# Kernel tuning notes

Hardware: AMD Instinct MI355X
Metric: run time of the kernel (lower is better)

Reference implementation:

```python
import jax, jax.numpy as jnp
import numpy as np
from jax import lax

HID, FFN, NUM_EXPERTS, TOP_K = 1024, 4096, 16, 4
B, S = 4, 2048


def setup_inputs() -> dict:
    key = jax.random.key(0)
    ks = jax.random.split(key, 7)
    scale = 0.02
    x = jax.random.normal(ks[0], (B, S, HID), dtype=jnp.float32)
    Wg = jax.random.normal(ks[1], (HID, NUM_EXPERTS), dtype=jnp.float32) * scale
    bg = jnp.zeros((NUM_EXPERTS,), dtype=jnp.float32)
    W1 = jax.random.normal(ks[2], (NUM_EXPERTS, HID, FFN), dtype=jnp.float32) * scale
    b1 = jnp.zeros((NUM_EXPERTS, FFN), dtype=jnp.float32)
    W2 = jax.random.normal(ks[3], (NUM_EXPERTS, FFN, HID), dtype=jnp.float32) * scale
    b2 = jnp.zeros((NUM_EXPERTS, HID), dtype=jnp.float32)
    return {"x": x, "Wg": Wg, "bg": bg, "W1": W1, "b1": b1, "W2": W2, "b2": b2}


def reference(x, Wg, bg, W1, b1, W2, b2):
    b, s, h = x.shape
    xf = x.reshape(-1, h)                                  # [T, H]
    T = xf.shape[0]
    logits = xf @ Wg + bg                                  # [T, E]
    top_w, top_idx = lax.top_k(logits, TOP_K)              # [T, K]
    top_w = jax.nn.softmax(top_w, axis=-1)
    # Dense combine weights [T, E]; topk indices are distinct so add == set.
    combine = jnp.zeros((T, NUM_EXPERTS), dtype=xf.dtype)
    combine = combine.at[jnp.arange(T)[:, None], top_idx].add(top_w)

    def body(acc, params):
        W1e, b1e, W2e, b2e, ce = params                    # ce: [T]
        hdn = jax.nn.gelu(xf @ W1e + b1e, approximate=False)  # [T, F]
        ye = hdn @ W2e + b2e                               # [T, H]
        return acc + ce[:, None] * ye, None

    out, _ = lax.scan(body, jnp.zeros_like(xf), (W1, b1, W2, b2, combine.T))
    return out.reshape(b, s, h)
```

## Files before the change

### kernel.cpp

```cpp
#include <hip/hip_runtime.h>
#include <hip/hip_bf16.h>


#define HID 1024
#define FFN 4096
#define NE 16
#define TOPK 4
#define NTOK 8192
#define NPAIR (NTOK*TOPK)

typedef __attribute__((ext_vector_type(4))) float f32x4;
typedef __attribute__((ext_vector_type(8))) short bf16x8;
typedef unsigned short u16;
typedef unsigned int u32;

__device__ __forceinline__ u16 f2bf(float f){
  u32 u = __float_as_uint(f);
  u32 r = (u + 0x7fffu + ((u >> 16) & 1u)) >> 16;
  return (u16)r;
}

__device__ __forceinline__ void gload_lds16(const void* g, void* l){
  __builtin_amdgcn_global_load_lds((const __attribute__((address_space(1))) void*)g,
                                   (__attribute__((address_space(3))) void*)l, 16, 0, 0);
}

__global__ __launch_bounds__(256) void k_gating(const float* __restrict__ x,
    const float* __restrict__ Wg, const float* __restrict__ bg,
    int* __restrict__ counts, int* __restrict__ tke, float* __restrict__ tkw,
    u16* __restrict__ xb){
  int t    = (blockIdx.x << 2) + (threadIdx.x >> 6);
  int lane = threadIdx.x & 63;
  const float* xr = x + (size_t)t*HID + lane*16;
  const float4* p = (const float4*)xr;
  float4 va = p[0], vb = p[1], vc = p[2], vd = p[3];
  float xv[16] = {va.x,va.y,va.z,va.w, vb.x,vb.y,vb.z,vb.w,
                  vc.x,vc.y,vc.z,vc.w, vd.x,vd.y,vd.z,vd.w};
  float acc[NE];
  #pragma unroll
  for (int e=0;e<NE;e++) acc[e] = 0.f;
  #pragma unroll
  for (int j=0;j<16;j++){
    const float* wr = Wg + (size_t)(lane*16 + j)*NE;
    #pragma unroll
    for (int e=0;e<NE;e++) acc[e] += xv[j] * wr[e];
  }
  uint4 o0, o1;
  o0.x = (u32)f2bf(xv[0])  | ((u32)f2bf(xv[1])  << 16);
  o0.y = (u32)f2bf(xv[2])  | ((u32)f2bf(xv[3])  << 16);
  o0.z = (u32)f2bf(xv[4])  | ((u32)f2bf(xv[5])  << 16);
  o0.w = (u32)f2bf(xv[6])  | ((u32)f2bf(xv[7])  << 16);
  o1.x = (u32)f2bf(xv[8])  | ((u32)f2bf(xv[9])  << 16);
  o1.y = (u32)f2bf(xv[10]) | ((u32)f2bf(xv[11]) << 16);
  o1.z = (u32)f2bf(xv[12]) | ((u32)f2bf(xv[13]) << 16);
  o1.w = (u32)f2bf(xv[14]) | ((u32)f2bf(xv[15]) << 16);
  u16* xbr = xb + (size_t)t*HID + lane*16;
  *(uint4*)xbr       = o0;
  *(uint4*)(xbr + 8) = o1;

  #pragma unroll
  for (int off=32; off; off>>=1){
    #pragma unroll
    for (int e=0;e<NE;e++) acc[e] += __shfl_xor(acc[e], off);
  }
  if (lane == 0){
    #pragma unroll
    for (int e=0;e<NE;e++) acc[e] += bg[e];
    int te[TOPK]; float tv[TOPK];
    #pragma unroll
    for (int k=0;k<TOPK;k++){
      int bi = 0; float bv = -1e30f;
      #pragma unroll
      for (int e=0;e<NE;e++) if (acc[e] > bv){ bv = acc[e]; bi = e; }
      te[k] = bi; tv[k] = bv; acc[bi] = -1e30f;
    }
    float m = tv[0], s = 0.f, w[TOPK];
    #pragma unroll
    for (int k=0;k<TOPK;k++){ w[k] = expf(tv[k]-m); s += w[k]; }
    float inv = 1.f/s;
    #pragma unroll
    for (int k=0;k<TOPK;k++){
      tke[t*TOPK+k] = te[k];
      tkw[t*TOPK+k] = w[k]*inv;
      atomicAdd(&counts[te[k]], 1);
    }
  }
}

__global__ __launch_bounds__(256) void k_scatter(const int* __restrict__ tke,
    const float* __restrict__ tkw, const int* __restrict__ counts,
    int* __restrict__ offsets, int* __restrict__ cursors,
    int* __restrict__ ltok, float* __restrict__ lw){
  __shared__ int loff[NE+1];
  if (threadIdx.x == 0){
    int a = 0;
    for (int e=0;e<NE;e++){ loff[e] = a; a += counts[e]; }
    loff[NE] = a;
    if (blockIdx.x == 0){
      for (int e=0;e<=NE;e++) offsets[e] = loff[e];
    }
  }
  __syncthreads();
  int t = blockIdx.x*256 + threadIdx.x;
  #pragma unroll
  for (int k=0;k<TOPK;k++){
    int e = tke[t*TOPK+k];
    int p = atomicAdd(&cursors[e], 1);
    int r = loff[e] + p;
    ltok[r] = t;
    lw[r]   = tkw[t*TOPK+k];
  }
}

__global__ __launch_bounds__(256) void k_wcvt(const float* __restrict__ src,
    u16* __restrict__ dst, int R, int C){
  int ntR = R >> 6, ntC = C >> 7;
  int ntiles = NE * ntR * ntC;
  __shared__ u16 t[64][136];
  int tid = threadIdx.x;
  for (int tile = blockIdx.x; tile < ntiles; tile += gridDim.x){
    int e   = tile / (ntR*ntC);
    int rem = tile % (ntR*ntC);
    int rt  = rem / ntC, ct = rem % ntC;
    const float* s = src + (size_t)e*R*C + (size_t)(rt*64)*C + ct*128;
    u16*         d = dst + (size_t)e*R*C + (size_t)(ct*128)*R + rt*64;
    #pragma unroll
    for (int it=0; it<8; it++){
      int i  = it*256 + tid;
      int rr = i >> 5;
      int c4 = (i & 31) << 2;
      float4 v = *(const float4*)(s + (size_t)rr*C + c4);
      t[rr][c4+0] = f2bf(v.x);
      t[rr][c4+1] = f2bf(v.y);
      t[rr][c4+2] = f2bf(v.z);
      t[rr][c4+3] = f2bf(v.w);
    }
    __syncthreads();
    #pragma unroll
    for (int it=0; it<4; it++){
      int i   = it*256 + tid;
      int cc  = i >> 3;
      int rr0 = (i & 7) << 3;
      uint4 o;
      o.x = (u32)t[rr0+0][cc] | ((u32)t[rr0+1][cc] << 16);
      o.y = (u32)t[rr0+2][cc] | ((u32)t[rr0+3][cc] << 16);
      o.z = (u32)t[rr0+4][cc] | ((u32)t[rr0+5][cc] << 16);
      o.w = (u32)t[rr0+6][cc] | ((u32)t[rr0+7][cc] << 16);
      *(uint4*)(d + (size_t)cc*R + rr0) = o;
    }
    __syncthreads();
  }
}

__global__ __launch_bounds__(512, 2) void k_ffn1(
    const u16* __restrict__ xb, const u16* __restrict__ w1t,
    const float* __restrict__ b1,
    const int* __restrict__ counts, const int* __restrict__ offsets,
    const int* __restrict__ ltok, u16* __restrict__ hdn){
  int e = blockIdx.z;
  int cnt = counts[e];
  int row0 = blockIdx.y << 8;
  if (row0 >= cnt) return;
  int n0 = blockIdx.x << 8;
  int soff = offsets[e];
  const int* lt = ltok + soff;

  __shared__ u16 lA[2][256*64];
  __shared__ u16 lB[2][256*64];

  int tid = threadIdx.x, lane = tid & 63, wv = tid >> 6;
  int wr = (wv >> 2) << 7;
  int wc = (wv & 3) << 6;
  int l15 = lane & 15, lkhi = (lane >> 4) << 3;

  f32x4 acc[8][4];
  #pragma unroll
  for (int m=0;m<8;m++){
    #pragma unroll
    for (int n=0;n<4;n++) acc[m][n] = (f32x4)0.f;
  }
  const u16* wBp = w1t + ((size_t)e*FFN + n0)*HID;

  u32 aoff[4], boff[4];
  #pragma unroll
  for (int it=0; it<4; it++){
    int cidx = it*512 + tid;
    int row  = cidx >> 3;
    int kc   = ((cidx & 7) ^ (row & 7)) << 3;
    int rc = row0 + row; if (rc > cnt-1) rc = cnt-1;
    aoff[it] = (u32)lt[rc]*HID + kc;
    boff[it] = (u32)row*HID + kc;
  }

  auto stage = [&](int buf, int k0v){
    #pragma unroll
    for (int it=0; it<4; it++){
      int cidx = it*512 + tid;
      gload_lds16(xb  + aoff[it] + k0v, &lA[buf][cidx<<3]);
      gload_lds16(wBp + boff[it] + k0v, &lB[buf][cidx<<3]);
    }
  };

  stage(0, 0);
  __syncthreads();
  int cur = 0;
  for (int t=0; t<HID/64; ++t){
    if (t+1 < HID/64) stage(cur^1, (t+1)*64);
    #pragma unroll
    for (int kk=0; kk<64; kk+=32){
      bf16x8 af[8], bfv[4];
      #pragma unroll
      for (int m=0;m<8;m++){
        int ra = wr + m*16 + l15;
        af[m]  = *(const bf16x8*)&lA[cur][ra*64 + ((kk + lkhi) ^ ((ra&7)<<3))];
      }
      #pragma unroll
      for (int n=0;n<4;n++){
        int rb = wc + n*16 + l15;
        bfv[n] = *(const bf16x8*)&lB[cur][rb*64 + ((kk + lkhi) ^ ((rb&7)<<3))];
      }
      #pragma unroll
      for (int m=0;m<8;m++){
        #pragma unroll
        for (int n=0;n<4;n++)
          acc[m][n] = __builtin_amdgcn_mfma_f32_16x16x32_bf16(af[m], bfv[n], acc[m][n], 0,0,0);
      }
    }
    __syncthreads();
    cur ^= 1;
  }
  int rhi = (lane >> 4) << 2;
  #pragma unroll
  for (int m=0;m<8;m++){
    int rl = wr + m*16 + rhi;
    #pragma unroll
    for (int j=0;j<4;j++){
      int row = row0 + rl + j;
      if (row < cnt){
        size_t base = (size_t)(soff + row)*FFN;
        #pragma unroll
        for (int n=0;n<4;n++){
          int col = n0 + wc + n*16 + l15;
          float z = acc[m][n][j] + b1[(size_t)e*FFN + col];
          float g = 0.5f*z*(1.0f + erff(z*0.70710678118654752f));
          hdn[base + col] = f2bf(g);
        }
      }
    }
  }
}

__global__ __launch_bounds__(512, 2) void k_ffn2(
    const u16* __restrict__ hdn, const u16* __restrict__ w2t,
    const float* __restrict__ b2,
    const int* __restrict__ counts, const int* __restrict__ offsets,
    const int* __restrict__ ltok, const float* __restrict__ lw,
    float* __restrict__ out){
  int e = blockIdx.z;
  int cnt = counts[e];
  int row0 = blockIdx.y << 8;
  if (row0 >= cnt) return;
  int n0 = blockIdx.x << 8;
  int soff = offsets[e];

  __shared__ u16 lA[2][256*64];
  __shared__ u16 lB[2][256*64];

  int tid = threadIdx.x, lane = tid & 63, wv = tid >> 6;
  int wr = (wv >> 2) << 7;
  int wc = (wv & 3) << 6;
  int l15 = lane & 15, lkhi = (lane >> 4) << 3;

  f32x4 acc[8][4];
  #pragma unroll
  for (int m=0;m<8;m++){
    #pragma unroll
    for (int n=0;n<4;n++) acc[m][n] = (f32x4)0.f;
  }
  const u16* wBp = w2t + ((size_t)e*HID + n0)*FFN;

  u32 aoff[4], boff[4];
  #pragma unroll
  for (int it=0; it<4; it++){
    int cidx = it*512 + tid;
    int row  = cidx >> 3;
    int kc   = ((cidx & 7) ^ (row & 7)) << 3;
    int rc = row0 + row; if (rc > cnt-1) rc = cnt-1;
    aoff[it] = (u32)(soff+rc)*FFN + kc;
    boff[it] = (u32)row*FFN + kc;
  }

  auto stage = [&](int buf, int k0v){
    #pragma unroll
    for (int it=0; it<4; it++){
      int cidx = it*512 + tid;
      gload_lds16(hdn + aoff[it] + k0v, &lA[buf][cidx<<3]);
      gload_lds16(wBp + boff[it] + k0v, &lB[buf][cidx<<3]);
    }
  };

  stage(0, 0);
  __syncthreads();
  int cur = 0;
  for (int t=0; t<FFN/64; ++t){
    if (t+1 < FFN/64) stage(cur^1, (t+1)*64);
    #pragma unroll
    for (int kk=0; kk<64; kk+=32){
      bf16x8 af[8], bfv[4];
      #pragma unroll
      for (int m=0;m<8;m++){
        int ra = wr + m*16 + l15;
        af[m]  = *(const bf16x8*)&lA[cur][ra*64 + ((kk + lkhi) ^ ((ra&7)<<3))];
      }
      #pragma unroll
      for (int n=0;n<4;n++){
        int rb = wc + n*16 + l15;
        bfv[n] = *(const bf16x8*)&lB[cur][rb*64 + ((kk + lkhi) ^ ((rb&7)<<3))];
      }
      #pragma unroll
      for (int m=0;m<8;m++){
        #pragma unroll
        for (int n=0;n<4;n++)
          acc[m][n] = __builtin_amdgcn_mfma_f32_16x16x32_bf16(af[m], bfv[n], acc[m][n], 0,0,0);
      }
    }
    __syncthreads();
    cur ^= 1;
  }
  int rhi = (lane >> 4) << 2;
  #pragma unroll
  for (int m=0;m<8;m++){
    int rl = wr + m*16 + rhi;
    #pragma unroll
    for (int j=0;j<4;j++){
      int row = row0 + rl + j;
      if (row < cnt){
        float sw = lw[soff+row];
        int tok  = ltok[soff+row];
        float* orow = out + (size_t)tok*HID;
        #pragma unroll
        for (int n=0;n<4;n++){
          int col = n0 + wc + n*16 + l15;
          atomicAdd(orow + col, sw*(acc[m][n][j] + b2[(size_t)e*HID + col]));
        }
      }
    }
  }
}

extern "C" void kernel_launch(void* const* d_in, const int* in_sizes, int n_in,
                              void* d_out, int out_size, void* d_ws, size_t ws_size,
                              hipStream_t stream){
  const float* x  = (const float*)d_in[0];
  const float* Wg = (const float*)d_in[1];
  const float* bg = (const float*)d_in[2];
  const float* W1 = (const float*)d_in[3];
  const float* b1 = (const float*)d_in[4];
  const float* W2 = (const float*)d_in[5];
  const float* b2 = (const float*)d_in[6];
  float* out = (float*)d_out;

  char* ws = (char*)d_ws;
  size_t off = 0;
  u16* SLOT_A = (u16*)(ws + off); off += (size_t)NE*FFN*HID*2;
  u16* XB  = (u16*)(ws + off); off += (size_t)NTOK*HID*2;
  u16* HDN = (u16*)(ws + off); off += (size_t)NPAIR*FFN*2;
  int*   LTOK = (int*)(ws + off);   off += (size_t)NPAIR*4;
  float* LW   = (float*)(ws + off); off += (size_t)NPAIR*4;
  int*   TKE  = (int*)(ws + off);   off += (size_t)NPAIR*4;
  float* TKW  = (float*)(ws + off); off += (size_t)NPAIR*4;
  int*   CTRL = (int*)(ws + off);   off += 256;
  int* counts  = CTRL;
  int* offsets = CTRL + 16;
  int* cursors = CTRL + 33;

  (void)hipMemsetAsync(CTRL, 0, 256, stream);
  (void)hipMemsetAsync(out, 0, (size_t)NTOK*HID*sizeof(float), stream);

  k_gating<<<NTOK/4, 256, 0, stream>>>(x, Wg, bg, counts, TKE, TKW, XB);
  k_scatter<<<NTOK/256, 256, 0, stream>>>(TKE, TKW, counts, offsets, cursors, LTOK, LW);
  k_wcvt<<<2048, 256, 0, stream>>>(W1, SLOT_A, HID, FFN);
  k_ffn1<<<dim3(FFN/256, NTOK/256, NE), 512, 0, stream>>>(XB, SLOT_A, b1, counts, offsets, LTOK, HDN);
  k_wcvt<<<2048, 256, 0, stream>>>(W2, SLOT_A, FFN, HID);
  k_ffn2<<<dim3(HID/256, NTOK/256, NE), 512, 0, stream>>>(HDN, SLOT_A, b2, counts, offsets, LTOK, LW, out);
}
```

Before: 2.248 ms.

## Use persistent grid with compacted expert tile list for FFN GEMMs

Replaces the dense 3D grid (N-tiles x max row-tiles x experts), which launched many blocks that exit immediately, with a fixed 256-block persistent grid. Each block builds a prefix sum over per-expert row-tile counts and loops over only the valid (expert, row-tile, col-tile) work items. This removes the cost of scheduling empty blocks and packs real work onto the CUs. In exchange, each block pays for a prefix scan and an expert search per item, and the static stride assignment can leave the CUs unevenly loaded.

Result: faster. 2.193 ms (-2.4%).

```diff
diff --git a/kernel.cpp b/kernel.cpp
--- a/kernel.cpp
+++ b/kernel.cpp
@@ -157,14 +157,6 @@
     const float* __restrict__ b1,
     const int* __restrict__ counts, const int* __restrict__ offsets,
     const int* __restrict__ ltok, u16* __restrict__ hdn){
-  int e = blockIdx.z;
-  int cnt = counts[e];
-  int row0 = blockIdx.y << 8;
-  if (row0 >= cnt) return;
-  int n0 = blockIdx.x << 8;
-  int soff = offsets[e];
-  const int* lt = ltok + soff;
-
   __shared__ u16 lA[2][256*64];
   __shared__ u16 lB[2][256*64];
 
@@ -172,78 +164,100 @@
   int wr = (wv >> 2) << 7;
   int wc = (wv & 3) << 6;
   int l15 = lane & 15, lkhi = (lane >> 4) << 3;
-
-  f32x4 acc[8][4];
-  #pragma unroll
-  for (int m=0;m<8;m++){
-    #pragma unroll
-    for (int n=0;n<4;n++) acc[m][n] = (f32x4)0.f;
-  }
-  const u16* wBp = w1t + ((size_t)e*FFN + n0)*HID;
-
-  u32 aoff[4], boff[4];
-  #pragma unroll
-  for (int it=0; it<4; it++){
-    int cidx = it*512 + tid;
-    int row  = cidx >> 3;
-    int kc   = ((cidx & 7) ^ (row & 7)) << 3;
-    int rc = row0 + row; if (rc > cnt-1) rc = cnt-1;
-    aoff[it] = (u32)lt[rc]*HID + kc;
-    boff[it] = (u32)row*HID + kc;
-  }
-
-  auto stage = [&](int buf, int k0v){
+  int rhi = (lane >> 4) << 2;
+
+  const int NTN = FFN >> 8;
+  int pref[NE+1];
+  {
+    int a = 0;
+    #pragma unroll
+    for (int e=0;e<NE;e++){ pref[e] = a; a += ((counts[e] + 255) >> 8) * NTN; }
+    pref[NE] = a;
+  }
+  int tot = pref[NE];
+
+  for (int item = blockIdx.x; item < tot; item += gridDim.x){
+    int e = 0;
+    #pragma unroll
+    for (int q=0;q<NE;q++) if (item >= pref[q+1]) e = q+1;
+    int loc = item - pref[e];
+    int rt = loc / NTN, nt = loc % NTN;
+    int cnt = counts[e];
+    int row0 = rt << 8, n0 = nt << 8;
+    int soff = offsets[e];
+    const int* lt = ltok + soff;
+    const u16* wBp = w1t + ((size_t)e*FFN + n0)*HID;
+
+    f32x4 acc[8][4];
+    #pragma unroll
+    for (int m=0;m<8;m++){
+      #pragma unroll
+      for (int n=0;n<4;n++) acc[m][n] = (f32x4)0.f;
+    }
+
+    u32 aoff[4], boff[4];
     #pragma unroll
     for (int it=0; it<4; it++){
       int cidx = it*512 + tid;
-      gload_lds16(xb  + aoff[it] + k0v, &lA[buf][cidx<<3]);
-      gload_lds16(wBp + boff[it] + k0v, &lB[buf][cidx<<3]);
-    }
-  };
-
-  stage(0, 0);
-  __syncthreads();
-  int cur = 0;
-  for (int t=0; t<HID/64; ++t){
-    if (t+1 < HID/64) stage(cur^1, (t+1)*64);
-    #pragma unroll
-    for (int kk=0; kk<64; kk+=32){
-      bf16x8 af[8], bfv[4];
-      #pragma unroll
-      for (int m=0;m<8;m++){
-        int ra = wr + m*16 + l15;
-        af[m]  = *(const bf16x8*)&lA[cur][ra*64 + ((kk + lkhi) ^ ((ra&7)<<3))];
-      }
-      #pragma unroll
-      for (int n=0;n<4;n++){
-        int rb = wc + n*16 + l15;
-        bfv[n] = *(const bf16x8*)&lB[cur][rb*64 + ((kk + lkhi) ^ ((rb&7)<<3))];
-      }
-      #pragma unroll
-      for (int m=0;m<8;m++){
-        #pragma unroll
-        for (int n=0;n<4;n++)
-          acc[m][n] = __builtin_amdgcn_mfma_f32_16x16x32_bf16(af[m], bfv[n], acc[m][n], 0,0,0);
-      }
-    }
+      int row  = cidx >> 3;
+      int kc   = ((cidx & 7) ^ (row & 7)) << 3;
+      int rc = row0 + row; if (rc > cnt-1) rc = cnt-1;
+      aoff[it] = (u32)lt[rc]*HID + kc;
+      boff[it] = (u32)row*HID + kc;
+    }
+
+    auto stage = [&](int buf, int k0v){
+      #pragma unroll
+      for (int it=0; it<4; it++){
+        int cidx = it*512 + tid;
+        gload_lds16(xb  + aoff[it] + k0v, &lA[buf][cidx<<3]);
+        gload_lds16(wBp + boff[it] + k0v, &lB[buf][cidx<<3]);
+      }
+    };
+
+    stage(0, 0);
     __syncthreads();
-    cur ^= 1;
-  }
-  int rhi = (lane >> 4) << 2;
-  #pragma unroll
-  for (int m=0;m<8;m++){
-    int rl = wr + m*16 + rhi;
-    #pragma unroll
-    for (int j=0;j<4;j++){
-      int row = row0 + rl + j;
-      if (row < cnt){
-        size_t base = (size_t)(soff + row)*FFN;
+    int cur = 0;
+    for (int t=0; t<HID/64; ++t){
+      if (t+1 < HID/64) stage(cur^1, (t+1)*64);
+      #pragma unroll
+      for (int kk=0; kk<64; kk+=32){
+        bf16x8 af[8], bfv[4];
+        #pragma unroll
+        for (int m=0;m<8;m++){
+          int ra = wr + m*16 + l15;
+          af[m]  = *(const bf16x8*)&lA[cur][ra*64 + ((kk + lkhi) ^ ((ra&7)<<3))];
+        }
         #pragma unroll
         for (int n=0;n<4;n++){
-          int col = n0 + wc + n*16 + l15;
-          float z = acc[m][n][j] + b1[(size_t)e*FFN + col];
-          float g = 0.5f*z*(1.0f + erff(z*0.70710678118654752f));
-          hdn[base + col] = f2bf(g);
+          int rb = wc + n*16 + l15;
+          bfv[n] = *(const bf16x8*)&lB[cur][rb*64 + ((kk + lkhi) ^ ((rb&7)<<3))];
+        }
+        #pragma unroll
+        for (int m=0;m<8;m++){
+          #pragma unroll
+          for (int n=0;n<4;n++)
+            acc[m][n] = __builtin_amdgcn_mfma_f32_16x16x32_bf16(af[m], bfv[n], acc[m][n], 0,0,0);
+        }
+      }
+      __syncthreads();
+      cur ^= 1;
+    }
+    #pragma unroll
+    for (int m=0;m<8;m++){
+      int rl = wr + m*16 + rhi;
+      #pragma unroll
+      for (int j=0;j<4;j++){
+        int row = row0 + rl + j;
+        if (row < cnt){
+          size_t base = (size_t)(soff + row)*FFN;
+          #pragma unroll
+          for (int n=0;n<4;n++){
+            int col = n0 + wc + n*16 + l15;
+            float z = acc[m][n][j] + b1[(size_t)e*FFN + col];
+            float g = 0.5f*z*(1.0f + erff(z*0.70710678118654752f));
+            hdn[base + col] = f2bf(g);
+          }
         }
       }
     }
@@ -256,13 +270,6 @@
     const int* __restrict__ counts, const int* __restrict__ offsets,
     const int* __restrict__ ltok, const float* __restrict__ lw,
     float* __restrict__ out){
-  int e = blockIdx.z;
-  int cnt = counts[e];
-  int row0 = blockIdx.y << 8;
-  if (row0 >= cnt) return;
-  int n0 = blockIdx.x << 8;
-  int soff = offsets[e];
-
   __shared__ u16 lA[2][256*64];
   __shared__ u16 lB[2][256*64];
 
@@ -270,78 +277,99 @@
   int wr = (wv >> 2) << 7;
   int wc = (wv & 3) << 6;
   int l15 = lane & 15, lkhi = (lane >> 4) << 3;
-
-  f32x4 acc[8][4];
-  #pragma unroll
-  for (int m=0;m<8;m++){
-    #pragma unroll
-    for (int n=0;n<4;n++) acc[m][n] = (f32x4)0.f;
-  }
-  const u16* wBp = w2t + ((size_t)e*HID + n0)*FFN;
-
-  u32 aoff[4], boff[4];
-  #pragma unroll
-  for (int it=0; it<4; it++){
-    int cidx = it*512 + tid;
-    int row  = cidx >> 3;
-    int kc   = ((cidx & 7) ^ (row & 7)) << 3;
-    int rc = row0 + row; if (rc > cnt-1) rc = cnt-1;
-    aoff[it] = (u32)(soff+rc)*FFN + kc;
-    boff[it] = (u32)row*FFN + kc;
-  }
-
-  auto stage = [&](int buf, int k0v){
+  int rhi = (lane >> 4) << 2;
+
+  const int NTN = HID >> 8;
+  int pref[NE+1];
+  {
+    int a = 0;
+    #pragma unroll
+    for (int e=0;e<NE;e++){ pref[e] = a; a += ((counts[e] + 255) >> 8) * NTN; }
+    pref[NE] = a;
+  }
+  int tot = pref[NE];
+
+  for (int item = blockIdx.x; item < tot; item += gridDim.x){
+    int e = 0;
+    #pragma unroll
+    for (int q=0;q<NE;q++) if (item >= pref[q+1]) e = q+1;
+    int loc = item - pref[e];
+    int rt = loc / NTN, nt = loc % NTN;
+    int cnt = counts[e];
+    int row0 = rt << 8, n0 = nt << 8;
+    int soff = offsets[e];
+    const u16* wBp = w2t + ((size_t)e*HID + n0)*FFN;
+
+    f32x4 acc[8][4];
+    #pragma unroll
+    for (int m=0;m<8;m++){
+      #pragma unroll
+      for (int n=0;n<4;n++) acc[m][n] = (f32x4)0.f;
+    }
+
+    u32 aoff[4], boff[4];
     #pragma unroll
     for (int it=0; it<4; it++){
       int cidx = it*512 + tid;
-      gload_lds16(hdn + aoff[it] + k0v, &lA[buf][cidx<<3]);
-      gload_lds16(wBp + boff[it] + k0v, &lB[buf][cidx<<3]);
-    }
-  };
-
-  stage(0, 0);
-  __syncthreads();
-  int cur = 0;
-  for (int t=0; t<FFN/64; ++t){
-    if (t+1 < FFN/64) stage(cur^1, (t+1)*64);
-    #pragma unroll
-    for (int kk=0; kk<64; kk+=32){
-      bf16x8 af[8], bfv[4];
-      #pragma unroll
-      for (int m=0;m<8;m++){
-        int ra = wr + m*16 + l15;
-        af[m]  = *(const bf16x8*)&lA[cur][ra*64 + ((kk + lkhi) ^ ((ra&7)<<3))];
-      }
-      #pragma unroll
-      for (int n=0;n<4;n++){
-        int rb = wc + n*16 + l15;
-        bfv[n] = *(const bf16x8*)&lB[cur][rb*64 + ((kk + lkhi) ^ ((rb&7)<<3))];
-      }
-      #pragma unroll
-      for (int m=0;m<8;m++){
-        #pragma unroll
-        for (int n=0;n<4;n++)
-          acc[m][n] = __builtin_amdgcn_mfma_f32_16x16x32_bf16(af[m], bfv[n], acc[m][n], 0,0,0);
-      }
-    }
+      int row  = cidx >> 3;
+      int kc   = ((cidx & 7) ^ (row & 7)) << 3;
+      int rc = row0 + row; if (rc > cnt-1) rc = cnt-1;
+      aoff[it] = (u32)(soff+rc)*FFN + kc;
+      boff[it] = (u32)row*FFN + kc;
+    }
+
+    auto stage = [&](int buf, int k0v){
+      #pragma unroll
+      for (int it=0; it<4; it++){
+        int cidx = it*512 + tid;
+        gload_lds16(hdn + aoff[it] + k0v, &lA[buf][cidx<<3]);
+        gload_lds16(wBp + boff[it] + k0v, &lB[buf][cidx<<3]);
+      }
+    };
+
+    stage(0, 0);
     __syncthreads();
-    cur ^= 1;
-  }
-  int rhi = (lane >> 4) << 2;
-  #pragma unroll
-  for (int m=0;m<8;m++){
-    int rl = wr + m*16 + rhi;
-    #pragma unroll
-    for (int j=0;j<4;j++){
-      int row = row0 + rl + j;
-      if (row < cnt){
-        float sw = lw[soff+row];
-        int tok  = ltok[soff+row];
-        float* orow = out + (size_t)tok*HID;
+    int cur = 0;
+    for (int t=0; t<FFN/64; ++t){
+      if (t+1 < FFN/64) stage(cur^1, (t+1)*64);
+      #pragma unroll
+      for (int kk=0; kk<64; kk+=32){
+        bf16x8 af[8], bfv[4];
+        #pragma unroll
+        for (int m=0;m<8;m++){
+          int ra = wr + m*16 + l15;
+          af[m]  = *(const bf16x8*)&lA[cur][ra*64 + ((kk + lkhi) ^ ((ra&7)<<3))];
+        }
         #pragma unroll
         for (int n=0;n<4;n++){
-          int col = n0 + wc + n*16 + l15;
-          atomicAdd(orow + col, sw*(acc[m][n][j] + b2[(size_t)e*HID + col]));
+          int rb = wc + n*16 + l15;
+          bfv[n] = *(const bf16x8*)&lB[cur][rb*64 + ((kk + lkhi) ^ ((rb&7)<<3))];
+        }
+        #pragma unroll
+        for (int m=0;m<8;m++){
+          #pragma unroll
+          for (int n=0;n<4;n++)
+            acc[m][n] = __builtin_amdgcn_mfma_f32_16x16x32_bf16(af[m], bfv[n], acc[m][n], 0,0,0);
+        }
+      }
+      __syncthreads();
+      cur ^= 1;
+    }
+    #pragma unroll
+    for (int m=0;m<8;m++){
+      int rl = wr + m*16 + rhi;
+      #pragma unroll
+      for (int j=0;j<4;j++){
+        int row = row0 + rl + j;
+        if (row < cnt){
+          float sw = lw[soff+row];
+          int tok  = ltok[soff+row];
+          float* orow = out + (size_t)tok*HID;
+          #pragma unroll
+          for (int n=0;n<4;n++){
+            int col = n0 + wc + n*16 + l15;
+            atomicAdd(orow + col, sw*(acc[m][n][j] + b2[(size_t)e*HID + col]));
+          }
         }
       }
     }
@@ -380,7 +408,7 @@
   k_gating<<<NTOK/4, 256, 0, stream>>>(x, Wg, bg, counts, TKE, TKW, XB);
   k_scatter<<<NTOK/256, 256, 0, stream>>>(TKE, TKW, counts, offsets, cursors, LTOK, LW);
   k_wcvt<<<2048, 256, 0, stream>>>(W1, SLOT_A, HID, FFN);
-  k_ffn1<<<dim3(FFN/256, NTOK/256, NE), 512, 0, stream>>>(XB, SLOT_A, b1, counts, offsets, LTOK, HDN);
+  k_ffn1<<<256, 512, 0, stream>>>(XB, SLOT_A, b1, counts, offsets, LTOK, HDN);
   k_wcvt<<<2048, 256, 0, stream>>>(W2, SLOT_A, FFN, HID);
-  k_ffn2<<<dim3(HID/256, NTOK/256, NE), 512, 0, stream>>>(HDN, SLOT_A, b2, counts, offsets, LTOK, LW, out);
-}
+  k_ffn2<<<256, 512, 0, stream>>>(HDN, SLOT_A, b2, counts, offsets, LTOK, LW, out);
+}
```
